# Performance work log

Measured on AMD Instinct MI355X. Metric: run time of the kernel, lower is better.

The kernel has to match this reference:

```python
import jax, jax.numpy as jnp
import numpy as np

N = 50000
IN_DIM = 128
HID = 16
HEADS = 8
NUM_CLASSES = 16
NEG_SLOPE = 0.2


def _glorot(key, shape):
    fan_in, fan_out = shape[0], shape[-1]
    lim = float(np.sqrt(6.0 / (fan_in + fan_out)))
    return jax.random.uniform(key, shape, jnp.float32, -lim, lim)


def setup_inputs() -> dict:
    key = jax.random.key(0)
    ks = jax.random.split(key, 12)
    x = jax.random.normal(ks[0], (N, IN_DIM), jnp.float32)
    edge_index = jax.random.randint(ks[1], (2, 1600000), 0, N, jnp.int64)
    # conv1: in=IN_DIM, out per head=HID, heads=HEADS
    Wl1 = _glorot(ks[2], (IN_DIM, HEADS * HID))
    Wr1 = _glorot(ks[3], (IN_DIM, HEADS * HID))
    att1 = _glorot(ks[4], (HEADS, HID))
    b1 = jnp.zeros((HEADS * HID,), jnp.float32)
    # conv2: in=HID*HEADS, out per head=NUM_CLASSES
    Wl2 = _glorot(ks[5], (HEADS * HID, HEADS * NUM_CLASSES))
    Wr2 = _glorot(ks[6], (HEADS * HID, HEADS * NUM_CLASSES))
    att2 = _glorot(ks[7], (HEADS, NUM_CLASSES))
    b2 = jnp.zeros((HEADS * NUM_CLASSES,), jnp.float32)
    # final linear: NUM_CLASSES*HEADS -> NUM_CLASSES
    Wlin = _glorot(ks[8], (HEADS * NUM_CLASSES, NUM_CLASSES))
    blin = jnp.zeros((NUM_CLASSES,), jnp.float32)
    return dict(x=x, edge_index=edge_index, Wl1=Wl1, Wr1=Wr1, att1=att1, b1=b1,
                Wl2=Wl2, Wr2=Wr2, att2=att2, b2=b2, Wlin=Wlin, blin=blin)


def _gatv2_conv(x, src, dst, Wl, Wr, att, bias, heads, out_ch):
    n = x.shape[0]
    xl = (x @ Wl).reshape(n, heads, out_ch)  # source transform
    xr = (x @ Wr).reshape(n, heads, out_ch)  # target transform
    # additive attention logits per edge (GATv2)
    e = jax.nn.leaky_relu(xl[src] + xr[dst], NEG_SLOPE)          # [E,H,C]
    logits = jnp.einsum('ehc,hc->eh', e, att)                     # [E,H]
    # per-destination segment softmax
    m = jax.ops.segment_max(logits, dst, num_segments=n)          # [N,H]
    a = jnp.exp(logits - m[dst])                                  # [E,H]
    s = jax.ops.segment_sum(a, dst, num_segments=n)               # [N,H]
    alpha = a / (s[dst] + 1e-16)
    out = jax.ops.segment_sum(alpha[:, :, None] * xl[src], dst, num_segments=n)
    return out.reshape(n, heads * out_ch) + bias


def reference(x, edge_index, Wl1, Wr1, att1, b1, Wl2, Wr2, att2, b2, Wlin, blin):
    n = x.shape[0]
    # add self-loops (PyG GATv2Conv default add_self_loops=True)
    loop = jnp.arange(n, dtype=edge_index.dtype)
    src = jnp.concatenate([edge_index[0], loop])
    dst = jnp.concatenate([edge_index[1], loop])
    h = _gatv2_conv(x, src, dst, Wl1, Wr1, att1, b1, HEADS, HID)
    h = jax.nn.relu(h)  # dropout identity in eval mode
    h = _gatv2_conv(h, src, dst, Wl2, Wr2, att2, b2, HEADS, NUM_CLASSES)
    h = jax.nn.relu(h)
    logits = h @ Wlin + blin
    return jax.nn.log_softmax(logits, axis=1)
```

## Files before the change

### kernel.cpp

```cpp
#include <hip/hip_runtime.h>

#define HEADS 8
#define FDIM 128
#define NCLS 16
#define NEG_SLOPE 0.2f
#define LOG2E 1.4426950408889634f

typedef __attribute__((ext_vector_type(8))) short bf16x8;
typedef __attribute__((ext_vector_type(4))) float f32x4;

__device__ __forceinline__ unsigned short f2bf(float f) {
    unsigned u = __float_as_uint(f);
    unsigned r = u + 0x7FFFu + ((u >> 16) & 1u);
    return (unsigned short)(r >> 16);
}

__global__ __launch_bounds__(256) void gemm_csr(const float* __restrict__ Xf,
                                                const unsigned short* __restrict__ Xb,
                                                const float* __restrict__ W0,
                                                const float* __restrict__ W1,
                                                unsigned short* __restrict__ Y0,
                                                unsigned short* __restrict__ Y1,
                                                int n,
                                                const int* __restrict__ srcs,
                                                const int* __restrict__ dsts,
                                                int* __restrict__ cnt,
                                                int* __restrict__ adj,
                                                int E0, int pad, int GB, int SB) {
    __shared__ __align__(16) unsigned short ws[8 * 4 * 64 * 8];
    __shared__ __align__(16) unsigned short ys[64 * 132];
    const int t = threadIdx.x;
    const int x = blockIdx.x;
    int gIdx;
    if (SB > 0) {
        if ((x % 5) == 4) {
            int i = (x / 5) * 256 + t;
            const int stride = SB * 256;
            for (; i < E0; i += stride) {
                const int d = dsts[i];
                const int rk = atomicAdd(&cnt[d], 1);
                if (rk < pad) adj[(size_t)d * pad + rk] = srcs[i];
            }
            return;
        }
        gIdx = (x / 5) * 4 + (x % 5);
    } else {
        gIdx = x;
    }
    if (gIdx >= 2 * GB) return;
    const int side = (gIdx >= GB) ? 1 : 0;
    const float* W = side ? W1 : W0;
    unsigned short* Y = side ? Y1 : Y0;
    const int nb = (side ? gIdx - GB : gIdx) * 64;

#pragma unroll
    for (int i = 0; i < 16; i++) {
        const int f = t + i * 256;
        const int k = f >> 5, n4 = f & 31;
        const float4 v = *(const float4*)(W + k * 128 + n4 * 4);
        const int kc = k >> 5, q = (k >> 3) & 3, j = k & 7;
        const float vv[4] = {v.x, v.y, v.z, v.w};
#pragma unroll
        for (int e = 0; e < 4; e++) {
            const int nn = n4 * 4 + e;
            ws[((((nn >> 4) * 4 + kc) * 64 + q * 16 + (nn & 15)) << 3) + j] = f2bf(vv[e]);
        }
    }
    __syncthreads();

    const int w = t >> 6, lane = t & 63;
    const int q = lane >> 4, jd = lane & 15;
    const bf16x8* wb = (const bf16x8*)ws;

    const int row = nb + w * 16 + jd;
    bf16x8 bx[4];
#pragma unroll
    for (int kc = 0; kc < 4; kc++) bx[kc] = (bf16x8){0,0,0,0,0,0,0,0};
    if (row < n) {
        if (Xb) {
            const unsigned short* xp = Xb + (size_t)row * 128 + q * 8;
#pragma unroll
            for (int kc = 0; kc < 4; kc++) bx[kc] = *(const bf16x8*)(xp + kc * 32);
        } else {
            const float* xp = Xf + (size_t)row * 128 + q * 8;
#pragma unroll
            for (int kc = 0; kc < 4; kc++) {
                const float4 v0 = *(const float4*)(xp + kc * 32);
                const float4 v1 = *(const float4*)(xp + kc * 32 + 4);
                union { unsigned short us[8]; bf16x8 b; } pk;
                pk.us[0] = f2bf(v0.x); pk.us[1] = f2bf(v0.y);
                pk.us[2] = f2bf(v0.z); pk.us[3] = f2bf(v0.w);
                pk.us[4] = f2bf(v1.x); pk.us[5] = f2bf(v1.y);
                pk.us[6] = f2bf(v1.z); pk.us[7] = f2bf(v1.w);
                bx[kc] = pk.b;
            }
        }
    }
    f32x4 acc[8];
#pragma unroll
    for (int i = 0; i < 8; i++) acc[i] = (f32x4){0.f, 0.f, 0.f, 0.f};
#pragma unroll
    for (int kc = 0; kc < 4; kc++) {
#pragma unroll
        for (int ct = 0; ct < 8; ct++)
            acc[ct] = __builtin_amdgcn_mfma_f32_16x16x32_bf16(
                wb[(ct * 4 + kc) * 64 + lane], bx[kc], acc[ct], 0, 0, 0);
    }
    {
        unsigned short* yrow = ys + (w * 16 + jd) * 132;
#pragma unroll
        for (int ct = 0; ct < 8; ct++) {
            union { unsigned short us[4]; uint2 u2; } pk;
            pk.us[0] = f2bf(acc[ct][0]); pk.us[1] = f2bf(acc[ct][1]);
            pk.us[2] = f2bf(acc[ct][2]); pk.us[3] = f2bf(acc[ct][3]);
            *(uint2*)(yrow + ct * 16 + q * 4) = pk.u2;
        }
    }
    {
        const int rr = lane >> 4;
        const int ch = lane & 15;
#pragma unroll
        for (int i = 0; i < 4; i++) {
            const int lrow = w * 16 + i * 4 + rr;
            const int grow = nb + lrow;
            const uint4 v = *(const uint4*)(ys + lrow * 132 + ch * 8);
            if (grow < n)
                *(uint4*)(Y + (size_t)grow * 128 + ch * 8) = v;
        }
    }
}

#define GATHER_EDGE4(SRC, GATE)                                              \
    {                                                                        \
        const uint4 lv_ = *(const uint4*)(xl + (size_t)(SRC) * FDIM + col);  \
        const float l0_ = __uint_as_float(lv_.x << 16);                      \
        const float l1_ = __uint_as_float(lv_.x & 0xFFFF0000u);              \
        const float l2_ = __uint_as_float(lv_.y << 16);                      \
        const float l3_ = __uint_as_float(lv_.y & 0xFFFF0000u);              \
        const float l4_ = __uint_as_float(lv_.z << 16);                      \
        const float l5_ = __uint_as_float(lv_.z & 0xFFFF0000u);              \
        const float l6_ = __uint_as_float(lv_.w << 16);                      \
        const float l7_ = __uint_as_float(lv_.w & 0xFFFF0000u);              \
        float z_, p_;                                                        \
        z_ = l0_ + r0; z_ = fmaxf(z_, NEG_SLOPE * z_); p_  = z_ * a0;        \
        z_ = l1_ + r1; z_ = fmaxf(z_, NEG_SLOPE * z_); p_ += z_ * a1;        \
        z_ = l2_ + r2; z_ = fmaxf(z_, NEG_SLOPE * z_); p_ += z_ * a2;        \
        z_ = l3_ + r3; z_ = fmaxf(z_, NEG_SLOPE * z_); p_ += z_ * a3;        \
        z_ = l4_ + r4; z_ = fmaxf(z_, NEG_SLOPE * z_); p_ += z_ * a4;        \
        z_ = l5_ + r5; z_ = fmaxf(z_, NEG_SLOPE * z_); p_ += z_ * a5;        \
        z_ = l6_ + r6; z_ = fmaxf(z_, NEG_SLOPE * z_); p_ += z_ * a6;        \
        z_ = l7_ + r7; z_ = fmaxf(z_, NEG_SLOPE * z_); p_ += z_ * a7;        \
        p_ += __shfl_xor(p_, 1, 64);                                         \
        const float e_ = exp2f(p_ - mx) * (GATE);                            \
        s += e_;                                                             \
        c0 += e_ * l0_; c1 += e_ * l1_; c2 += e_ * l2_; c3 += e_ * l3_;      \
        c4 += e_ * l4_; c5 += e_ * l5_; c6 += e_ * l6_; c7 += e_ * l7_;      \
    }

template <bool HEAD>
__global__ __launch_bounds__(256) void node_gather(const unsigned short* __restrict__ xl,
                                                   const unsigned short* __restrict__ xr,
                                                   const float* __restrict__ att,
                                                   const int* __restrict__ adj,
                                                   const int* __restrict__ cnt,
                                                   const float* __restrict__ bias,
                                                   unsigned short* __restrict__ outC,
                                                   const float* __restrict__ headW,
                                                   const float* __restrict__ headB,
                                                   float* __restrict__ outH,
                                                   int n, int pad) {
    __shared__ float WsL[HEAD ? FDIM * NCLS : 1];
    __shared__ __align__(16) float stage[HEAD ? 4 : 1][FDIM];
    const int t = threadIdx.x;
    if (HEAD) {
        for (int i = t; i < FDIM * NCLS; i += 256) WsL[i] = headW[i];
        __syncthreads();
    }
    const int lane = t & 63;
    const int w = t >> 6;
    const int node = blockIdx.x * 4 + w;
    if (node >= n) return;
    const int g = lane >> 4;
    const int sub = lane & 15;
    const int col = sub * 8;
    float a0, a1, a2, a3, a4, a5, a6, a7;
    {
        const float4 v0 = *(const float4*)(att + col);
        const float4 v1 = *(const float4*)(att + col + 4);
        a0 = v0.x * LOG2E; a1 = v0.y * LOG2E; a2 = v0.z * LOG2E; a3 = v0.w * LOG2E;
        a4 = v1.x * LOG2E; a5 = v1.y * LOG2E; a6 = v1.z * LOG2E; a7 = v1.w * LOG2E;
    }
    float r0, r1, r2, r3, r4, r5, r6, r7;
    float sl0, sl1, sl2, sl3, sl4, sl5, sl6, sl7;
    {
        const uint4 rv = *(const uint4*)(xr + (size_t)node * FDIM + col);
        r0 = __uint_as_float(rv.x << 16); r1 = __uint_as_float(rv.x & 0xFFFF0000u);
        r2 = __uint_as_float(rv.y << 16); r3 = __uint_as_float(rv.y & 0xFFFF0000u);
        r4 = __uint_as_float(rv.z << 16); r5 = __uint_as_float(rv.z & 0xFFFF0000u);
        r6 = __uint_as_float(rv.w << 16); r7 = __uint_as_float(rv.w & 0xFFFF0000u);
        const uint4 lv = *(const uint4*)(xl + (size_t)node * FDIM + col);
        sl0 = __uint_as_float(lv.x << 16); sl1 = __uint_as_float(lv.x & 0xFFFF0000u);
        sl2 = __uint_as_float(lv.y << 16); sl3 = __uint_as_float(lv.y & 0xFFFF0000u);
        sl4 = __uint_as_float(lv.z << 16); sl5 = __uint_as_float(lv.z & 0xFFFF0000u);
        sl6 = __uint_as_float(lv.w << 16); sl7 = __uint_as_float(lv.w & 0xFFFF0000u);
    }
    float mx;
    {
        float z, p;
        z = sl0 + r0; z = fmaxf(z, NEG_SLOPE * z); p  = z * a0;
        z = sl1 + r1; z = fmaxf(z, NEG_SLOPE * z); p += z * a1;
        z = sl2 + r2; z = fmaxf(z, NEG_SLOPE * z); p += z * a2;
        z = sl3 + r3; z = fmaxf(z, NEG_SLOPE * z); p += z * a3;
        z = sl4 + r4; z = fmaxf(z, NEG_SLOPE * z); p += z * a4;
        z = sl5 + r5; z = fmaxf(z, NEG_SLOPE * z); p += z * a5;
        z = sl6 + r6; z = fmaxf(z, NEG_SLOPE * z); p += z * a6;
        z = sl7 + r7; z = fmaxf(z, NEG_SLOPE * z); p += z * a7;
        p += __shfl_xor(p, 1, 64);
        mx = p;
    }
    float s, c0, c1, c2, c3, c4, c5, c6, c7;
    if (g == 0) { s = 1.f; c0 = sl0; c1 = sl1; c2 = sl2; c3 = sl3;
                  c4 = sl4; c5 = sl5; c6 = sl6; c7 = sl7; }
    else        { s = 0.f; c0 = c1 = c2 = c3 = c4 = c5 = c6 = c7 = 0.f; }

    const int* ap = adj + (size_t)node * pad;
    const int deg = min(cnt[node], pad);
    int j = 0;
    for (; j + 8 <= deg; j += 8) {
        const int e0 = ap[j + g];
        const int e1 = ap[j + 4 + g];
        GATHER_EDGE4(e0, 1.f)
        GATHER_EDGE4(e1, 1.f)
    }
    for (; j < deg; j += 4) {
        const int idx = j + g;
        const int e0 = (idx < deg) ? ap[idx] : ap[deg - 1];
        const float gate = (idx < deg) ? 1.f : 0.f;
        GATHER_EDGE4(e0, gate)
    }
    s  += __shfl_xor(s, 16, 64);  s  += __shfl_xor(s, 32, 64);
    c0 += __shfl_xor(c0, 16, 64); c0 += __shfl_xor(c0, 32, 64);
    c1 += __shfl_xor(c1, 16, 64); c1 += __shfl_xor(c1, 32, 64);
    c2 += __shfl_xor(c2, 16, 64); c2 += __shfl_xor(c2, 32, 64);
    c3 += __shfl_xor(c3, 16, 64); c3 += __shfl_xor(c3, 32, 64);
    c4 += __shfl_xor(c4, 16, 64); c4 += __shfl_xor(c4, 32, 64);
    c5 += __shfl_xor(c5, 16, 64); c5 += __shfl_xor(c5, 32, 64);
    c6 += __shfl_xor(c6, 16, 64); c6 += __shfl_xor(c6, 32, 64);
    c7 += __shfl_xor(c7, 16, 64); c7 += __shfl_xor(c7, 32, 64);

    const float inv = 1.f / (s + 1e-16f);
    float o0, o1, o2, o3, o4, o5, o6, o7;
    {
        const float4 b0 = *(const float4*)(bias + col);
        const float4 b1 = *(const float4*)(bias + col + 4);
        o0 = fmaxf(c0 * inv + b0.x, 0.f); o1 = fmaxf(c1 * inv + b0.y, 0.f);
        o2 = fmaxf(c2 * inv + b0.z, 0.f); o3 = fmaxf(c3 * inv + b0.w, 0.f);
        o4 = fmaxf(c4 * inv + b1.x, 0.f); o5 = fmaxf(c5 * inv + b1.y, 0.f);
        o6 = fmaxf(c6 * inv + b1.z, 0.f); o7 = fmaxf(c7 * inv + b1.w, 0.f);
    }

    if (!HEAD) {
        if (g == 0) {
            union { unsigned short us[8]; uint4 u4; } pk;
            pk.us[0] = f2bf(o0); pk.us[1] = f2bf(o1);
            pk.us[2] = f2bf(o2); pk.us[3] = f2bf(o3);
            pk.us[4] = f2bf(o4); pk.us[5] = f2bf(o5);
            pk.us[6] = f2bf(o6); pk.us[7] = f2bf(o7);
            *(uint4*)(outC + (size_t)node * FDIM + col) = pk.u4;
        }
        return;
    }
    if (g == 0) {
        *(float4*)&stage[w][col]     = make_float4(o0, o1, o2, o3);
        *(float4*)&stage[w][col + 4] = make_float4(o4, o5, o6, o7);
    }
    const int cls = lane & 15;
    const int q = lane >> 4;
    float acc = 0.f;
#pragma unroll
    for (int k = 0; k < 32; k++)
        acc += stage[w][q * 32 + k] * WsL[(q * 32 + k) * NCLS + cls];
    acc += __shfl_xor(acc, 16, 64);
    acc += __shfl_xor(acc, 32, 64);
    acc += headB[cls];
    float m2 = acc;
    m2 = fmaxf(m2, __shfl_xor(m2, 8, 64));
    m2 = fmaxf(m2, __shfl_xor(m2, 4, 64));
    m2 = fmaxf(m2, __shfl_xor(m2, 2, 64));
    m2 = fmaxf(m2, __shfl_xor(m2, 1, 64));
    float sm = __expf(acc - m2);
    sm += __shfl_xor(sm, 8, 64);
    sm += __shfl_xor(sm, 4, 64);
    sm += __shfl_xor(sm, 2, 64);
    sm += __shfl_xor(sm, 1, 64);
    if (lane < 16)
        outH[(size_t)node * NCLS + cls] = acc - m2 - __logf(sm);
}

extern "C" void kernel_launch(void* const* d_in, const int* in_sizes, int n_in,
                              void* d_out, int out_size, void* d_ws, size_t ws_size,
                              hipStream_t stream) {
    const float* x    = (const float*)d_in[0];
    const int*   edge = (const int*)d_in[1];
    const float* Wl1  = (const float*)d_in[2];
    const float* Wr1  = (const float*)d_in[3];
    const float* att1 = (const float*)d_in[4];
    const float* b1   = (const float*)d_in[5];
    const float* Wl2  = (const float*)d_in[6];
    const float* Wr2  = (const float*)d_in[7];
    const float* att2 = (const float*)d_in[8];
    const float* b2   = (const float*)d_in[9];
    const float* Wlin = (const float*)d_in[10];
    const float* blin = (const float*)d_in[11];

    const int N = in_sizes[0] / FDIM;
    const int E0 = in_sizes[1] / 2;
    const int* srcs = edge;
    const int* dsts = edge + E0;

    int PAD = 96;
    {
        size_t need = (size_t)3 * N * FDIM * 2 + (size_t)N * 4 + (size_t)N * PAD * 4;
        if (need > ws_size) PAD = 72;
    }

    unsigned short* A = (unsigned short*)d_ws;
    unsigned short* B = A + (size_t)N * FDIM;
    unsigned short* C = B + (size_t)N * FDIM;
    int* cnt   = (int*)(C + (size_t)N * FDIM);
    int* adj   = cnt + N;

    const int GB = (N + 63) / 64;
    const int G  = 2 * GB;
    const int SB = (G + 3) / 4;
    const int node_blocks = (N + 3) / 4;

    hipMemsetAsync(cnt, 0, (size_t)N * sizeof(int), stream);

    gemm_csr<<<5 * SB, 256, 0, stream>>>(
        x, nullptr, Wl1, Wr1, A, B, N, srcs, dsts, cnt, adj, E0, PAD, GB, SB);
    node_gather<false><<<node_blocks, 256, 0, stream>>>(
        A, B, att1, adj, cnt, b1, C, nullptr, nullptr, nullptr, N, PAD);

    gemm_csr<<<G, 256, 0, stream>>>(
        nullptr, C, Wl2, Wr2, A, B, N, nullptr, nullptr, nullptr, nullptr, 0, PAD, GB, 0);
    node_gather<true><<<node_blocks, 256, 0, stream>>>(
        A, B, att2, adj, cnt, b2, nullptr, Wlin, blin, (float*)d_out, N, PAD);
}
```

Baseline: 365.5 us.

## Pre-swizzle bf16 weights once, loop gemm blocks over multiple tiles, drop LDS staging

A new prep kernel converts all four weight matrices to the swizzled bf16 MFMA layout once and zeroes the CSR counters, replacing the memset. Each gemm block now copies the pre-swizzled weights into LDS and loops over two 64-row tiles (GB halved), so the fp32-to-bf16 weight conversion is amortised. Outputs are written straight from registers instead of being staged through an LDS transpose buffer. The trade-off is an extra kernel launch, fewer gemm blocks (and a different split of edge-scatter blocks, since SB is derived from GB), and narrower, less coalesced 8-byte global stores.

New measurement: 363.2 us. No clear change (-0.6%).

```diff
diff --git a/kernel.cpp b/kernel.cpp
--- a/kernel.cpp
+++ b/kernel.cpp
@@ -15,10 +15,40 @@
     return (unsigned short)(r >> 16);
 }
 
+__global__ __launch_bounds__(256) void prep(const float* __restrict__ W0,
+                                            const float* __restrict__ W1,
+                                            const float* __restrict__ W2,
+                                            const float* __restrict__ W3,
+                                            unsigned short* __restrict__ O,
+                                            int* __restrict__ cnt, int n) {
+    const int b = blockIdx.x;
+    const int t = threadIdx.x;
+    if (b < 4) {
+        const float* W = b == 0 ? W0 : b == 1 ? W1 : b == 2 ? W2 : W3;
+        unsigned short* out = O + b * 16384;
+#pragma unroll
+        for (int i = 0; i < 16; i++) {
+            const int f = t + i * 256;
+            const int k = f >> 5, n4 = f & 31;
+            const float4 v = *(const float4*)(W + k * 128 + n4 * 4);
+            const int kc = k >> 5, q = (k >> 3) & 3, j = k & 7;
+            const float vv[4] = {v.x, v.y, v.z, v.w};
+#pragma unroll
+            for (int e = 0; e < 4; e++) {
+                const int nn = n4 * 4 + e;
+                out[((((nn >> 4) * 4 + kc) * 64 + q * 16 + (nn & 15)) << 3) + j] = f2bf(vv[e]);
+            }
+        }
+        return;
+    }
+    const int stride = (gridDim.x - 4) * 256;
+    for (int i = (b - 4) * 256 + t; i < n; i += stride) cnt[i] = 0;
+}
+
 __global__ __launch_bounds__(256) void gemm_csr(const float* __restrict__ Xf,
                                                 const unsigned short* __restrict__ Xb,
-                                                const float* __restrict__ W0,
-                                                const float* __restrict__ W1,
+                                                const unsigned short* __restrict__ Wsw0,
+                                                const unsigned short* __restrict__ Wsw1,
                                                 unsigned short* __restrict__ Y0,
                                                 unsigned short* __restrict__ Y1,
                                                 int n,
@@ -28,7 +58,6 @@
                                                 int* __restrict__ adj,
                                                 int E0, int pad, int GB, int SB) {
     __shared__ __align__(16) unsigned short ws[8 * 4 * 64 * 8];
-    __shared__ __align__(16) unsigned short ys[64 * 132];
     const int t = threadIdx.x;
     const int x = blockIdx.x;
     int gIdx;
@@ -49,83 +78,68 @@
     }
     if (gIdx >= 2 * GB) return;
     const int side = (gIdx >= GB) ? 1 : 0;
-    const float* W = side ? W1 : W0;
+    const unsigned short* Wsw = side ? Wsw1 : Wsw0;
     unsigned short* Y = side ? Y1 : Y0;
-    const int nb = (side ? gIdx - GB : gIdx) * 64;
-
-#pragma unroll
-    for (int i = 0; i < 16; i++) {
-        const int f = t + i * 256;
-        const int k = f >> 5, n4 = f & 31;
-        const float4 v = *(const float4*)(W + k * 128 + n4 * 4);
-        const int kc = k >> 5, q = (k >> 3) & 3, j = k & 7;
-        const float vv[4] = {v.x, v.y, v.z, v.w};
-#pragma unroll
-        for (int e = 0; e < 4; e++) {
-            const int nn = n4 * 4 + e;
-            ws[((((nn >> 4) * 4 + kc) * 64 + q * 16 + (nn & 15)) << 3) + j] = f2bf(vv[e]);
-        }
+    const int bid = side ? gIdx - GB : gIdx;
+
+    {
+        const uint4* Wv = (const uint4*)Wsw;
+        uint4* wv = (uint4*)ws;
+#pragma unroll
+        for (int i = 0; i < 8; i++) wv[t + i * 256] = Wv[t + i * 256];
     }
     __syncthreads();
 
     const int w = t >> 6, lane = t & 63;
     const int q = lane >> 4, jd = lane & 15;
     const bf16x8* wb = (const bf16x8*)ws;
-
-    const int row = nb + w * 16 + jd;
-    bf16x8 bx[4];
-#pragma unroll
-    for (int kc = 0; kc < 4; kc++) bx[kc] = (bf16x8){0,0,0,0,0,0,0,0};
-    if (row < n) {
-        if (Xb) {
-            const unsigned short* xp = Xb + (size_t)row * 128 + q * 8;
-#pragma unroll
-            for (int kc = 0; kc < 4; kc++) bx[kc] = *(const bf16x8*)(xp + kc * 32);
-        } else {
-            const float* xp = Xf + (size_t)row * 128 + q * 8;
-#pragma unroll
-            for (int kc = 0; kc < 4; kc++) {
-                const float4 v0 = *(const float4*)(xp + kc * 32);
-                const float4 v1 = *(const float4*)(xp + kc * 32 + 4);
-                union { unsigned short us[8]; bf16x8 b; } pk;
-                pk.us[0] = f2bf(v0.x); pk.us[1] = f2bf(v0.y);
-                pk.us[2] = f2bf(v0.z); pk.us[3] = f2bf(v0.w);
-                pk.us[4] = f2bf(v1.x); pk.us[5] = f2bf(v1.y);
-                pk.us[6] = f2bf(v1.z); pk.us[7] = f2bf(v1.w);
-                bx[kc] = pk.b;
+    const int Gh = (n + 63) >> 6;
+
+    for (int tile = bid; tile < Gh; tile += GB) {
+        const int nb = tile * 64;
+        const int row = nb + w * 16 + jd;
+        bf16x8 bx[4];
+#pragma unroll
+        for (int kc = 0; kc < 4; kc++) bx[kc] = (bf16x8){0,0,0,0,0,0,0,0};
+        if (row < n) {
+            if (Xb) {
+                const unsigned short* xp = Xb + (size_t)row * 128 + q * 8;
+#pragma unroll
+                for (int kc = 0; kc < 4; kc++) bx[kc] = *(const bf16x8*)(xp + kc * 32);
+            } else {
+                const float* xp = Xf + (size_t)row * 128 + q * 8;
+#pragma unroll
+                for (int kc = 0; kc < 4; kc++) {
+                    const float4 v0 = *(const float4*)(xp + kc * 32);
+                    const float4 v1 = *(const float4*)(xp + kc * 32 + 4);
+                    union { unsigned short us[8]; bf16x8 b; } pk;
+                    pk.us[0] = f2bf(v0.x); pk.us[1] = f2bf(v0.y);
+                    pk.us[2] = f2bf(v0.z); pk.us[3] = f2bf(v0.w);
+                    pk.us[4] = f2bf(v1.x); pk.us[5] = f2bf(v1.y);
+                    pk.us[6] = f2bf(v1.z); pk.us[7] = f2bf(v1.w);
+                    bx[kc] = pk.b;
+                }
             }
         }
-    }
-    f32x4 acc[8];
-#pragma unroll
-    for (int i = 0; i < 8; i++) acc[i] = (f32x4){0.f, 0.f, 0.f, 0.f};
-#pragma unroll
-    for (int kc = 0; kc < 4; kc++) {
-#pragma unroll
-        for (int ct = 0; ct < 8; ct++)
-            acc[ct] = __builtin_amdgcn_mfma_f32_16x16x32_bf16(
-                wb[(ct * 4 + kc) * 64 + lane], bx[kc], acc[ct], 0, 0, 0);
-    }
-    {
-        unsigned short* yrow = ys + (w * 16 + jd) * 132;
-#pragma unroll
-        for (int ct = 0; ct < 8; ct++) {
-            union { unsigned short us[4]; uint2 u2; } pk;
-            pk.us[0] = f2bf(acc[ct][0]); pk.us[1] = f2bf(acc[ct][1]);
-            pk.us[2] = f2bf(acc[ct][2]); pk.us[3] = f2bf(acc[ct][3]);
-            *(uint2*)(yrow + ct * 16 + q * 4) = pk.u2;
-        }
-    }
-    {
-        const int rr = lane >> 4;
-        const int ch = lane & 15;
-#pragma unroll
-        for (int i = 0; i < 4; i++) {
-            const int lrow = w * 16 + i * 4 + rr;
-            const int grow = nb + lrow;
-            const uint4 v = *(const uint4*)(ys + lrow * 132 + ch * 8);
-            if (grow < n)
-                *(uint4*)(Y + (size_t)grow * 128 + ch * 8) = v;
+        f32x4 acc[8];
+#pragma unroll
+        for (int i = 0; i < 8; i++) acc[i] = (f32x4){0.f, 0.f, 0.f, 0.f};
+#pragma unroll
+        for (int kc = 0; kc < 4; kc++) {
+#pragma unroll
+            for (int ct = 0; ct < 8; ct++)
+                acc[ct] = __builtin_amdgcn_mfma_f32_16x16x32_bf16(
+                    wb[(ct * 4 + kc) * 64 + lane], bx[kc], acc[ct], 0, 0, 0);
+        }
+        if (row < n) {
+            unsigned short* yp = Y + (size_t)row * 128 + q * 4;
+#pragma unroll
+            for (int ct = 0; ct < 8; ct++) {
+                union { unsigned short us[4]; uint2 u2; } pk;
+                pk.us[0] = f2bf(acc[ct][0]); pk.us[1] = f2bf(acc[ct][1]);
+                pk.us[2] = f2bf(acc[ct][2]); pk.us[3] = f2bf(acc[ct][3]);
+                *(uint2*)(yp + ct * 16) = pk.u2;
+            }
         }
     }
 }
@@ -320,7 +334,8 @@
 
     int PAD = 96;
     {
-        size_t need = (size_t)3 * N * FDIM * 2 + (size_t)N * 4 + (size_t)N * PAD * 4;
+        size_t need = (size_t)3 * N * FDIM * 2 + (size_t)N * 4 + (size_t)N * PAD * 4
+                    + 4 * 16384 * 2;
         if (need > ws_size) PAD = 72;
     }
 
@@ -329,21 +344,23 @@
     unsigned short* C = B + (size_t)N * FDIM;
     int* cnt   = (int*)(C + (size_t)N * FDIM);
     int* adj   = cnt + N;
-
-    const int GB = (N + 63) / 64;
+    unsigned short* Wsw = (unsigned short*)(adj + (size_t)N * PAD);
+
+    const int GB = (N + 127) / 128;
     const int G  = 2 * GB;
     const int SB = (G + 3) / 4;
     const int node_blocks = (N + 3) / 4;
 
-    hipMemsetAsync(cnt, 0, (size_t)N * sizeof(int), stream);
+    prep<<<4 + 64, 256, 0, stream>>>(Wl1, Wr1, Wl2, Wr2, Wsw, cnt, N);
 
     gemm_csr<<<5 * SB, 256, 0, stream>>>(
-        x, nullptr, Wl1, Wr1, A, B, N, srcs, dsts, cnt, adj, E0, PAD, GB, SB);
+        x, nullptr, Wsw, Wsw + 16384, A, B, N, srcs, dsts, cnt, adj, E0, PAD, GB, SB);
     node_gather<false><<<node_blocks, 256, 0, stream>>>(
         A, B, att1, adj, cnt, b1, C, nullptr, nullptr, nullptr, N, PAD);
 
     gemm_csr<<<G, 256, 0, stream>>>(
-        nullptr, C, Wl2, Wr2, A, B, N, nullptr, nullptr, nullptr, nullptr, 0, PAD, GB, 0);
+        nullptr, C, Wsw + 2 * 16384, Wsw + 3 * 16384, A, B, N,
+        nullptr, nullptr, nullptr, nullptr, 0, PAD, GB, 0);
     node_gather<true><<<node_blocks, 256, 0, stream>>>(
         A, B, att2, adj, cnt, b2, nullptr, Wlin, blin, (float*)d_out, N, PAD);
 }
```
